# Kernel optimization log

Measured on AMD Instinct MI355X. Metric: run time of the kernel, lower is better.

## Reference

```python
import jax, jax.numpy as jnp
import numpy as np

W1 = 7          # half window
W2 = 2 * W1 + 1 # window size = 15
H = 4           # num heads
DH = 64         # head dim
DO = H * DH     # 256


def setup_inputs() -> dict:
    key = jax.random.key(0)
    ks = jax.random.split(key, 7)
    B, T, D = 2, 4096, 768
    s = 1.0 / np.sqrt(D).astype(np.float32)
    inputs = jax.random.normal(ks[0], (B, T, D), dtype=jnp.float32)
    Wq = jax.random.normal(ks[1], (DO, D), dtype=jnp.float32) * s
    bq = jax.random.normal(ks[2], (DO,), dtype=jnp.float32) * s
    Wv = jax.random.normal(ks[3], (DO, D), dtype=jnp.float32) * s
    bv = jax.random.normal(ks[4], (DO,), dtype=jnp.float32) * s
    pos_emb = jax.random.normal(ks[5], (W2, D), dtype=jnp.float32)
    return {"inputs": inputs, "Wq": Wq, "bq": bq, "Wv": Wv, "bv": bv, "pos_emb": pos_emb}


def reference(inputs, Wq, bq, Wv, bv, pos_emb):
    # Faithful to the torch module: k uses the *query* projection (source bug),
    # no softmax, no 1/sqrt(d) scaling.
    B, T, D = inputs.shape
    pad = jnp.pad(inputs, ((0, 0), (W1, W1), (0, 0)))  # [B, T+2*W1, D]
    # Project once on the padded sequence, then gather windows (linear ops
    # commute with the window gather; position bias added post-projection).
    q_pad = pad @ Wq.T + bq            # [B, T+2*W1, DO]
    v_pad = pad @ Wv.T + bv            # [B, T+2*W1, DO]
    pos_q = pos_emb @ Wq.T             # [W2, DO]  (query(window+pos) = query(window)+pos@Wq^T)
    pos_v = pos_emb @ Wv.T             # [W2, DO]
    idx = jnp.arange(T)[:, None] + jnp.arange(W2)[None, :]  # [T, W2]
    k = q_pad[:, idx] + pos_q          # [B, T, W2, DO]
    v = v_pad[:, idx] + pos_v          # [B, T, W2, DO]
    q = inputs @ Wq.T + bq             # [B, T, DO]
    qh = q.reshape(B, T, H, DH)
    kh = k.reshape(B, T, W2, H, DH)
    vh = v.reshape(B, T, W2, H, DH)
    scores = jnp.einsum('bthd,btwhd->bthw', qh, kh)   # [B, T, H, W2] (no softmax)
    ctx = jnp.einsum('bthw,btwhd->bthd', scores, vh)  # [B, T, H, DH]
    return ctx.reshape(B, T, DO)
```

## Files before the change

kernel.cpp:

```cpp
#include <hip/hip_runtime.h>

#define TPC   4110
#define MROWS 8220
#define MTOT  8235
#define MPAD  8320
#define KD    768

typedef __attribute__((ext_vector_type(8))) short short8;
typedef __attribute__((ext_vector_type(4))) float f32x4;

#define LOAD_LDS16(gp, lp)                                                   \
  __builtin_amdgcn_global_load_lds(                                          \
      (const __attribute__((address_space(1))) void*)(gp),                   \
      (__attribute__((address_space(3))) void*)(lp), 16, 0, 0)

__device__ inline unsigned bfr(float x) {
  unsigned u = __float_as_uint(x);
  return (u + 0x7FFFu + ((u >> 16) & 1u)) >> 16;
}
__device__ inline unsigned pack2(float a, float b) {
  return bfr(a) | (bfr(b) << 16);
}
__device__ inline float bflo(unsigned u) { return __uint_as_float(u << 16); }
__device__ inline float bfhi(unsigned u) { return __uint_as_float(u & 0xffff0000u); }

__global__ __launch_bounds__(256) void cast_ab(
    const float* __restrict__ inp, const float* __restrict__ Wq,
    const float* __restrict__ Wv, const float* __restrict__ pos,
    ushort* __restrict__ Abf, ushort* __restrict__ Wbf) {
  const int ACH = MPAD * 96;
  int gid = blockIdx.x * 256 + threadIdx.x;
  const float* src = nullptr;
  ushort* dst;
  if (gid < ACH) {
    int row = gid / 96, c = (gid - row * 96) * 8;
    dst = Abf + (size_t)row * KD + c;
    if (row < MROWS) {
      int b = row / TPC, t = row - b * TPC - 7;
      if (t >= 0 && t < 4096) src = inp + ((size_t)b * 4096 + t) * KD + c;
    } else if (row < MTOT) {
      src = pos + (size_t)(row - MROWS) * KD + c;
    }
  } else {
    int wid = gid - ACH;
    if (wid >= 512 * 96) return;
    int row = wid / 96, c = (wid - row * 96) * 8;
    dst = Wbf + (size_t)row * KD + c;
    src = (row < 256) ? Wq + (size_t)row * KD + c
                      : Wv + (size_t)(row - 256) * KD + c;
  }
  uint4 o;
  if (src) {
    float4 f0 = *(const float4*)src;
    float4 f1 = *(const float4*)(src + 4);
    o.x = pack2(f0.x, f0.y); o.y = pack2(f0.z, f0.w);
    o.z = pack2(f1.x, f1.y); o.w = pack2(f1.z, f1.w);
  } else {
    o.x = o.y = o.z = o.w = 0u;
  }
  *(uint4*)dst = o;
}

__global__ __launch_bounds__(256) void gemm_bf16(
    const ushort* __restrict__ Abf, const ushort* __restrict__ Wbf,
    const float* __restrict__ bq, const float* __restrict__ bv,
    ushort* __restrict__ q_out, ushort* __restrict__ v_out,
    ushort* __restrict__ pos_q, ushort* __restrict__ pos_v) {
  __shared__ ushort Al[2][64 * 64];
  __shared__ ushort Bl[2][128 * 64];
  const int tid = threadIdx.x;
  const int wave = tid >> 6, lane = tid & 63;
  const int lin = blockIdx.x;
  const int wg = (lin & 7) * 65 + (lin >> 3);
  const int ns = wg & 3;
  const int m0 = (wg >> 2) * 64;
  const int wm = wave & 1, wn = wave >> 1;
  const int fr = lane & 15, quad = lane >> 4;

  const ushort* ag[2];
  #pragma unroll
  for (int i = 0; i < 2; i++) {
    int c = i * 256 + tid, row = c >> 3, kq = c & 7;
    ag[i] = Abf + (size_t)(m0 + row) * KD + ((kq ^ (row & 7)) * 8);
  }
  const ushort* bg[4];
  #pragma unroll
  for (int i = 0; i < 4; i++) {
    int c = i * 256 + tid, row = c >> 3, kq = c & 7;
    bg[i] = Wbf + (size_t)(ns * 128 + row) * KD + ((kq ^ (row & 7)) * 8);
  }

  f32x4 acc[2][4];
  #pragma unroll
  for (int i = 0; i < 2; i++)
    #pragma unroll
    for (int j = 0; j < 4; j++) acc[i][j] = 0.0f;

#define STAGE(b, k0)                                                         \
  do {                                                                       \
    _Pragma("unroll")                                                        \
    for (int i = 0; i < 2; i++)                                              \
      LOAD_LDS16(ag[i] + (k0), &Al[b][0] + (i * 256 + wave * 64) * 8);       \
    _Pragma("unroll")                                                        \
    for (int i = 0; i < 4; i++)                                              \
      LOAD_LDS16(bg[i] + (k0), &Bl[b][0] + (i * 256 + wave * 64) * 8);       \
  } while (0)

#define COMPUTE(b)                                                           \
  do {                                                                       \
    short8 afr[2][2], bfrag[2][4];                                           \
    _Pragma("unroll")                                                        \
    for (int ks = 0; ks < 2; ks++) {                                         \
      const int e = ((ks * 4 + quad) ^ (fr & 7)) * 8;        \
      _Pragma("unroll")                                                      \
      for (int i = 0; i < 2; i++)                                            \
        afr[ks][i] =                                                         \
            *(const short8*)(&Al[b][0] + (wm * 32 + i * 16 + fr) * 64 + e);  \
      _Pragma("unroll")                                                      \
      for (int j = 0; j < 4; j++)                                            \
        bfrag[ks][j] =                                                       \
            *(const short8*)(&Bl[b][0] + (wn * 64 + j * 16 + fr) * 64 + e);  \
    }                                                                        \
    _Pragma("unroll")                                                        \
    for (int ks = 0; ks < 2; ks++)                                           \
      _Pragma("unroll")                                                      \
      for (int i = 0; i < 2; i++)                                            \
        _Pragma("unroll")                                                    \
        for (int j = 0; j < 4; j++)                                          \
          acc[i][j] = __builtin_amdgcn_mfma_f32_16x16x32_bf16(               \
              afr[ks][i], bfrag[ks][j], acc[i][j], 0, 0, 0);                 \
  } while (0)

  STAGE(0, 0);
  __syncthreads();
  #pragma unroll 1
  for (int k0 = 0; k0 < 640; k0 += 128) {
    STAGE(1, k0 + 64);
    COMPUTE(0);
    __syncthreads();
    STAGE(0, k0 + 128);
    COMPUTE(1);
    __syncthreads();
  }
  STAGE(1, 704);
  COMPUTE(0);
  __syncthreads();
  COMPUTE(1);

#undef STAGE
#undef COMPUTE

  const float* bias = (ns < 2) ? bq : bv;
  ushort* outp = (ns < 2) ? q_out : v_out;
  ushort* posp = (ns < 2) ? pos_q : pos_v;
  const int wbase = (ns & 1) * 128;
  #pragma unroll
  for (int j = 0; j < 4; j++) {
    const int colq = wbase + wn * 64 + j * 16 + fr;
    const int h = colq >> 6, d = colq & 63;
    const float bj = bias[colq];
    #pragma unroll
    for (int i = 0; i < 2; i++) {
      const int mb = m0 + wm * 32 + i * 16 + quad * 4;
      #pragma unroll
      for (int r = 0; r < 4; r++) {
        const int m = mb + r;
        if (m < MROWS) {
          int b = m / TPC, tp = m - b * TPC;
          outp[(((size_t)(b * 4 + h)) * TPC + tp) * 64 + d] =
              (ushort)bfr(acc[i][j][r] + bj);
        } else if (m < MTOT) {
          posp[(m - MROWS) * 256 + colq] = (ushort)bfr(acc[i][j][r]);
        }
      }
    }
  }
}

__global__ __launch_bounds__(256) void win_attn4(
    const ushort* __restrict__ q_out, const ushort* __restrict__ v_out,
    const ushort* __restrict__ pos_q, const ushort* __restrict__ pos_v,
    float* __restrict__ out) {
  __shared__ __align__(16) float ks[78][68];
  __shared__ __align__(16) float vs[78][68];
  __shared__ __align__(16) float pq[15][68];
  __shared__ __align__(16) float pv[15][68];
  const int tid = threadIdx.x;
  const int bh = blockIdx.x >> 6, tile = blockIdx.x & 63;
  const int b = bh >> 2, h = bh & 3;
  const int t0 = tile * 64;

  const size_t slab = (((size_t)(b * 4 + h)) * TPC + t0) * 64;
  for (int idx = tid; idx < 624; idx += 256) {
    int row = idx >> 3, c8 = (idx & 7) * 8;
    uint4 kc = *(const uint4*)(q_out + slab + idx * 8);
    ks[row][c8 + 0] = bflo(kc.x); ks[row][c8 + 1] = bfhi(kc.x);
    ks[row][c8 + 2] = bflo(kc.y); ks[row][c8 + 3] = bfhi(kc.y);
    ks[row][c8 + 4] = bflo(kc.z); ks[row][c8 + 5] = bfhi(kc.z);
    ks[row][c8 + 6] = bflo(kc.w); ks[row][c8 + 7] = bfhi(kc.w);
    uint4 vc = *(const uint4*)(v_out + slab + idx * 8);
    vs[row][c8 + 0] = bflo(vc.x); vs[row][c8 + 1] = bfhi(vc.x);
    vs[row][c8 + 2] = bflo(vc.y); vs[row][c8 + 3] = bfhi(vc.y);
    vs[row][c8 + 4] = bflo(vc.z); vs[row][c8 + 5] = bfhi(vc.z);
    vs[row][c8 + 6] = bflo(vc.w); vs[row][c8 + 7] = bfhi(vc.w);
  }
  if (tid < 120) {
    int row = tid >> 3, c8 = (tid & 7) * 8;
    uint4 qc = *(const uint4*)(pos_q + row * 256 + h * 64 + c8);
    pq[row][c8 + 0] = bflo(qc.x); pq[row][c8 + 1] = bfhi(qc.x);
    pq[row][c8 + 2] = bflo(qc.y); pq[row][c8 + 3] = bfhi(qc.y);
    pq[row][c8 + 4] = bflo(qc.z); pq[row][c8 + 5] = bfhi(qc.z);
    pq[row][c8 + 6] = bflo(qc.w); pq[row][c8 + 7] = bfhi(qc.w);
    uint4 vc = *(const uint4*)(pos_v + row * 256 + h * 64 + c8);
    pv[row][c8 + 0] = bflo(vc.x); pv[row][c8 + 1] = bfhi(vc.x);
    pv[row][c8 + 2] = bflo(vc.y); pv[row][c8 + 3] = bfhi(vc.y);
    pv[row][c8 + 4] = bflo(vc.z); pv[row][c8 + 5] = bfhi(vc.z);
    pv[row][c8 + 6] = bflo(vc.w); pv[row][c8 + 7] = bfhi(vc.w);
  }
  __syncthreads();

  const int tl = tid >> 2, qtr = tid & 3, d0 = qtr * 16;
  float4 qv[4];
  #pragma unroll
  for (int c = 0; c < 4; c++) qv[c] = *(float4*)&ks[tl + 7][d0 + c * 4];
  float4 ctx[4];
  #pragma unroll
  for (int c = 0; c < 4; c++) ctx[c] = make_float4(0.f, 0.f, 0.f, 0.f);

  #pragma unroll
  for (int w = 0; w < 15; w++) {
    float p = 0.f;
    #pragma unroll
    for (int c = 0; c < 4; c++) {
      float4 kk = *(float4*)&ks[tl + w][d0 + c * 4];
      float4 pp = *(float4*)&pq[w][d0 + c * 4];
      p += qv[c].x * (kk.x + pp.x) + qv[c].y * (kk.y + pp.y) +
           qv[c].z * (kk.z + pp.z) + qv[c].w * (kk.w + pp.w);
    }
    p += __shfl_xor(p, 1, 64);
    p += __shfl_xor(p, 2, 64);
    #pragma unroll
    for (int c = 0; c < 4; c++) {
      float4 vv = *(float4*)&vs[tl + w][d0 + c * 4];
      float4 pp = *(float4*)&pv[w][d0 + c * 4];
      ctx[c].x += p * (vv.x + pp.x);
      ctx[c].y += p * (vv.y + pp.y);
      ctx[c].z += p * (vv.z + pp.z);
      ctx[c].w += p * (vv.w + pp.w);
    }
  }
  size_t oo = ((size_t)(b * 4096 + t0 + tl)) * 256 + h * 64 + d0;
  #pragma unroll
  for (int c = 0; c < 4; c++) *(float4*)(out + oo + c * 4) = ctx[c];
}

extern "C" void kernel_launch(void* const* d_in, const int* in_sizes, int n_in,
                              void* d_out, int out_size, void* d_ws,
                              size_t ws_size, hipStream_t stream) {
  const float* inp = (const float*)d_in[0];
  const float* Wq  = (const float*)d_in[1];
  const float* bq  = (const float*)d_in[2];
  const float* Wv  = (const float*)d_in[3];
  const float* bv  = (const float*)d_in[4];
  const float* pos = (const float*)d_in[5];
  float* out = (float*)d_out;

  char* ws = (char*)d_ws;
  ushort* Abf   = (ushort*)ws;
  ushort* Wbf   = (ushort*)(ws + 12779520);
  ushort* q_out = (ushort*)(ws + 13565952);
  ushort* v_out = (ushort*)(ws + 17774592);
  ushort* pos_q = (ushort*)(ws + 21983232);
  ushort* pos_v = (ushort*)(ws + 21990912);

  const int cast_chunks = MPAD * 96 + 512 * 96;
  hipLaunchKernelGGL(cast_ab, dim3(cast_chunks / 256), dim3(256), 0, stream,
                     inp, Wq, Wv, pos, Abf, Wbf);
  hipLaunchKernelGGL(gemm_bf16, dim3(520), dim3(256), 0, stream,
                     Abf, Wbf, bq, bv, q_out, v_out, pos_q, pos_v);
  hipLaunchKernelGGL(win_attn4, dim3(2 * 4 * 64), dim3(256), 0, stream,
                     q_out, v_out, pos_q, pos_v, out);
}
```

Before: 109.7 us.

## Fuse fp32-to-bf16 activation cast into GEMM A-tile staging

Removes the separate pass that cast the padded input and position embeddings to bf16 in workspace. The GEMM now loads fp32 activations into registers, converts them to bf16 and writes the swizzled tiles into LDS itself, while weights are still cast by a small kernel and loaded asynchronously. This avoids writing and re-reading a ~12.7MB bf16 buffer. In exchange, each A tile is read as fp32 four times (once per N-split block) and the A staging uses register loads plus LDS stores instead of direct global-to-LDS loads.

```diff
diff --git a/kernel.cpp b/kernel.cpp
--- a/kernel.cpp
+++ b/kernel.cpp
@@ -24,45 +24,24 @@
 __device__ inline float bflo(unsigned u) { return __uint_as_float(u << 16); }
 __device__ inline float bfhi(unsigned u) { return __uint_as_float(u & 0xffff0000u); }
 
-__global__ __launch_bounds__(256) void cast_ab(
-    const float* __restrict__ inp, const float* __restrict__ Wq,
-    const float* __restrict__ Wv, const float* __restrict__ pos,
-    ushort* __restrict__ Abf, ushort* __restrict__ Wbf) {
-  const int ACH = MPAD * 96;
+__global__ __launch_bounds__(256) void cast_w(
+    const float* __restrict__ Wq, const float* __restrict__ Wv,
+    ushort* __restrict__ Wbf) {
   int gid = blockIdx.x * 256 + threadIdx.x;
-  const float* src = nullptr;
-  ushort* dst;
-  if (gid < ACH) {
-    int row = gid / 96, c = (gid - row * 96) * 8;
-    dst = Abf + (size_t)row * KD + c;
-    if (row < MROWS) {
-      int b = row / TPC, t = row - b * TPC - 7;
-      if (t >= 0 && t < 4096) src = inp + ((size_t)b * 4096 + t) * KD + c;
-    } else if (row < MTOT) {
-      src = pos + (size_t)(row - MROWS) * KD + c;
-    }
-  } else {
-    int wid = gid - ACH;
-    if (wid >= 512 * 96) return;
-    int row = wid / 96, c = (wid - row * 96) * 8;
-    dst = Wbf + (size_t)row * KD + c;
-    src = (row < 256) ? Wq + (size_t)row * KD + c
-                      : Wv + (size_t)(row - 256) * KD + c;
-  }
+  int row = gid / 96, c = (gid - row * 96) * 8;
+  const float* src = (row < 256) ? Wq + (size_t)row * KD + c
+                                 : Wv + (size_t)(row - 256) * KD + c;
+  float4 f0 = *(const float4*)src;
+  float4 f1 = *(const float4*)(src + 4);
   uint4 o;
-  if (src) {
-    float4 f0 = *(const float4*)src;
-    float4 f1 = *(const float4*)(src + 4);
-    o.x = pack2(f0.x, f0.y); o.y = pack2(f0.z, f0.w);
-    o.z = pack2(f1.x, f1.y); o.w = pack2(f1.z, f1.w);
-  } else {
-    o.x = o.y = o.z = o.w = 0u;
-  }
-  *(uint4*)dst = o;
+  o.x = pack2(f0.x, f0.y); o.y = pack2(f0.z, f0.w);
+  o.z = pack2(f1.x, f1.y); o.w = pack2(f1.z, f1.w);
+  *(uint4*)(Wbf + (size_t)row * KD + c) = o;
 }
 
 __global__ __launch_bounds__(256) void gemm_bf16(
-    const ushort* __restrict__ Abf, const ushort* __restrict__ Wbf,
+    const float* __restrict__ inp, const float* __restrict__ pos,
+    const ushort* __restrict__ Wbf,
     const float* __restrict__ bq, const float* __restrict__ bv,
     ushort* __restrict__ q_out, ushort* __restrict__ v_out,
     ushort* __restrict__ pos_q, ushort* __restrict__ pos_v) {
@@ -77,11 +56,23 @@
   const int wm = wave & 1, wn = wave >> 1;
   const int fr = lane & 15, quad = lane >> 4;
 
-  const ushort* ag[2];
+  const float* agf[2];
+  int aoff[2];
   #pragma unroll
   for (int i = 0; i < 2; i++) {
     int c = i * 256 + tid, row = c >> 3, kq = c & 7;
-    ag[i] = Abf + (size_t)(m0 + row) * KD + ((kq ^ (row & 7)) * 8);
+    int m = m0 + row;
+    aoff[i] = c * 8;
+    const float* s = nullptr;
+    if (m < MROWS) {
+      int bb = (m >= TPC) ? 1 : 0;
+      int t = m - bb * TPC - 7;
+      if (t >= 0 && t < 4096)
+        s = inp + ((size_t)bb * 4096 + t) * KD + ((kq ^ (row & 7)) * 8);
+    } else if (m < MTOT) {
+      s = pos + (size_t)(m - MROWS) * KD + ((kq ^ (row & 7)) * 8);
+    }
+    agf[i] = s;
   }
   const ushort* bg[4];
   #pragma unroll
@@ -96,17 +87,43 @@
     #pragma unroll
     for (int j = 0; j < 4; j++) acc[i][j] = 0.0f;
 
-#define STAGE(b, k0)                                                         \
+  float4 fa[2][2];
+
+#define STAGE_A_LOAD(k0)                                                     \
   do {                                                                       \
     _Pragma("unroll")                                                        \
-    for (int i = 0; i < 2; i++)                                              \
-      LOAD_LDS16(ag[i] + (k0), &Al[b][0] + (i * 256 + wave * 64) * 8);       \
+    for (int i = 0; i < 2; i++) {                                            \
+      if (agf[i]) {                                                          \
+        fa[i][0] = *(const float4*)(agf[i] + (k0));                          \
+        fa[i][1] = *(const float4*)(agf[i] + (k0) + 4);                      \
+      } else {                                                               \
+        fa[i][0] = make_float4(0.f, 0.f, 0.f, 0.f);                         \
+        fa[i][1] = make_float4(0.f, 0.f, 0.f, 0.f);                         \
+      }                                                                      \
+    }                                                                        \
+  } while (0)
+
+#define STAGE_A_WRITE(bsel)                                                  \
+  do {                                                                       \
+    _Pragma("unroll")                                                        \
+    for (int i = 0; i < 2; i++) {                                            \
+      uint4 o;                                                               \
+      o.x = pack2(fa[i][0].x, fa[i][0].y);                                   \
+      o.y = pack2(fa[i][0].z, fa[i][0].w);                                   \
+      o.z = pack2(fa[i][1].x, fa[i][1].y);                                   \
+      o.w = pack2(fa[i][1].z, fa[i][1].w);                                   \
+      *(uint4*)(&Al[bsel][0] + aoff[i]) = o;                                 \
+    }                                                                        \
+  } while (0)
+
+#define STAGE_B(bsel, k0)                                                    \
+  do {                                                                       \
     _Pragma("unroll")                                                        \
     for (int i = 0; i < 4; i++)                                              \
-      LOAD_LDS16(bg[i] + (k0), &Bl[b][0] + (i * 256 + wave * 64) * 8);       \
+      LOAD_LDS16(bg[i] + (k0), &Bl[bsel][0] + (i * 256 + wave * 64) * 8);    \
   } while (0)
 
-#define COMPUTE(b)                                                           \
+#define COMPUTE(bsel)                                                        \
   do {                                                                       \
     short8 afr[2][2], bfrag[2][4];                                           \
     _Pragma("unroll")                                                        \
@@ -115,11 +132,11 @@
       _Pragma("unroll")                                                      \
       for (int i = 0; i < 2; i++)                                            \
         afr[ks][i] =                                                         \
-            *(const short8*)(&Al[b][0] + (wm * 32 + i * 16 + fr) * 64 + e);  \
+            *(const short8*)(&Al[bsel][0] + (wm * 32 + i * 16 + fr) * 64 + e);\
       _Pragma("unroll")                                                      \
       for (int j = 0; j < 4; j++)                                            \
         bfrag[ks][j] =                                                       \
-            *(const short8*)(&Bl[b][0] + (wn * 64 + j * 16 + fr) * 64 + e);  \
+            *(const short8*)(&Bl[bsel][0] + (wn * 64 + j * 16 + fr) * 64 + e);\
     }                                                                        \
     _Pragma("unroll")                                                        \
     for (int ks = 0; ks < 2; ks++)                                           \
@@ -131,23 +148,33 @@
               afr[ks][i], bfrag[ks][j], acc[i][j], 0, 0, 0);                 \
   } while (0)
 
-  STAGE(0, 0);
+  STAGE_A_LOAD(0);
+  STAGE_B(0, 0);
+  STAGE_A_WRITE(0);
   __syncthreads();
   #pragma unroll 1
   for (int k0 = 0; k0 < 640; k0 += 128) {
-    STAGE(1, k0 + 64);
+    STAGE_A_LOAD(k0 + 64);
+    STAGE_B(1, k0 + 64);
     COMPUTE(0);
+    STAGE_A_WRITE(1);
     __syncthreads();
-    STAGE(0, k0 + 128);
+    STAGE_A_LOAD(k0 + 128);
+    STAGE_B(0, k0 + 128);
     COMPUTE(1);
+    STAGE_A_WRITE(0);
     __syncthreads();
   }
-  STAGE(1, 704);
+  STAGE_A_LOAD(704);
+  STAGE_B(1, 704);
   COMPUTE(0);
+  STAGE_A_WRITE(1);
   __syncthreads();
   COMPUTE(1);
 
-#undef STAGE
+#undef STAGE_A_LOAD
+#undef STAGE_A_WRITE
+#undef STAGE_B
 #undef COMPUTE
 
   const float* bias = (ns < 2) ? bq : bv;
@@ -266,18 +293,15 @@
   float* out = (float*)d_out;
 
   char* ws = (char*)d_ws;
-  ushort* Abf   = (ushort*)ws;
-  ushort* Wbf   = (ushort*)(ws + 12779520);
-  ushort* q_out = (ushort*)(ws + 13565952);
-  ushort* v_out = (ushort*)(ws + 17774592);
-  ushort* pos_q = (ushort*)(ws + 21983232);
-  ushort* pos_v = (ushort*)(ws + 21990912);
-
-  const int cast_chunks = MPAD * 96 + 512 * 96;
-  hipLaunchKernelGGL(cast_ab, dim3(cast_chunks / 256), dim3(256), 0, stream,
-                     inp, Wq, Wv, pos, Abf, Wbf);
+  ushort* Wbf   = (ushort*)ws;
+  ushort* q_out = (ushort*)(ws + 786432);
+  ushort* v_out = (ushort*)(ws + 4995072);
+  ushort* pos_q = (ushort*)(ws + 9203712);
+  ushort* pos_v = (ushort*)(ws + 9211392);
+
+  hipLaunchKernelGGL(cast_w, dim3(192), dim3(256), 0, stream, Wq, Wv, Wbf);
   hipLaunchKernelGGL(gemm_bf16, dim3(520), dim3(256), 0, stream,
-                     Abf, Wbf, bq, bv, q_out, v_out, pos_q, pos_v);
+                     inp, pos, Wbf, bq, bv, q_out, v_out, pos_q, pos_v);
   hipLaunchKernelGGL(win_attn4, dim3(2 * 4 * 64), dim3(256), 0, stream,
                      q_out, v_out, pos_q, pos_v, out);
 }
```

New measurement: 107.9 us, median of 3. About the same (-1.6%).
